# Optimization experiments

Measured on AMD Instinct MI355X. Metric: run time of the kernel, lower is better.

Reference implementation:

```python
import jax, jax.numpy as jnp
import numpy as np

N_NODES = 1500
E = 48000
IN = 128
OUT = 32
HEADS = 4
EDIM = 16


def setup_inputs() -> dict:
    key = jax.random.key(0)
    ks = jax.random.split(key, 16)
    rn = lambda k, shape, s=0.1: jax.random.normal(k, shape, dtype=jnp.float32) * s
    return {
        "x": jax.random.normal(ks[0], (N_NODES, IN), dtype=jnp.float32),
        "edges": jax.random.randint(ks[1], (2, E), 0, N_NODES),
        "edge_feature": jax.random.normal(ks[2], (E, EDIM), dtype=jnp.float32),
        "W1": rn(ks[3], (IN, HEADS * OUT)),
        "att_src1": rn(ks[4], (HEADS, OUT)),
        "att_dst1": rn(ks[5], (HEADS, OUT)),
        "We": rn(ks[6], (EDIM, HEADS * OUT)),
        "att_e": rn(ks[7], (HEADS, OUT)),
        "b1": jnp.zeros((OUT,), jnp.float32),
        "W2": rn(ks[8], (OUT, HEADS * OUT)),
        "att_src2": rn(ks[9], (HEADS, OUT)),
        "att_dst2": rn(ks[10], (HEADS, OUT)),
        "b2": jnp.zeros((OUT,), jnp.float32),
        "fc1_w": rn(ks[11], (2 * OUT, 32)),
        "fc1_b": jnp.zeros((32,), jnp.float32),
        "fc2_w": rn(ks[12], (32, 2)),
        "fc2_b": jnp.zeros((2,), jnp.float32),
    }


def _gat(h, src, dst, n, a_src, a_dst, bias, extra_alpha=None):
    # h: [n, H, C] projected node features; edges j=src -> i=dst (PyG GATConv)
    alpha = (h * a_src).sum(-1)[src] + (h * a_dst).sum(-1)[dst]  # [Etot, H]
    if extra_alpha is not None:
        alpha = alpha + extra_alpha
    alpha = jax.nn.leaky_relu(alpha, negative_slope=0.2)
    m = jax.ops.segment_max(alpha, dst, num_segments=n)  # per-dst softmax (stable)
    e = jnp.exp(alpha - m[dst])
    s = jax.ops.segment_sum(e, dst, num_segments=n)
    w = e / s[dst]  # every node has a self loop -> denom > 0
    out = jax.ops.segment_sum(w[:, :, None] * h[src], dst, num_segments=n)  # [n, H, C]
    return out.mean(axis=1) + bias  # concat=False -> mean over heads


def reference(x, edges, edge_feature, W1, att_src1, att_dst1, We, att_e, b1,
              W2, att_src2, att_dst2, b2, fc1_w, fc1_b, fc2_w, fc2_b):
    n = x.shape[0]
    src0, dst0 = edges[0], edges[1]
    loop = jnp.arange(n, dtype=src0.dtype)
    src = jnp.concatenate([src0, loop])
    dst = jnp.concatenate([dst0, loop])
    # add_self_loops fill_value='mean': self-loop attr = mean of incoming edge attrs
    cnt = jax.ops.segment_sum(jnp.ones_like(dst0, dtype=jnp.float32), dst0, num_segments=n)
    loop_attr = jax.ops.segment_sum(edge_feature, dst0, num_segments=n) / jnp.maximum(cnt, 1.0)[:, None]
    ea = jnp.concatenate([edge_feature, loop_attr], axis=0)  # [E+n, EDIM]

    H, C = att_src1.shape
    # layer 1: GATConv with edge features
    h1 = (x @ W1).reshape(n, H, C)
    extra = ((ea @ We).reshape(-1, H, C) * att_e).sum(-1)  # [E+n, H]
    x1 = _gat(h1, src, dst, n, att_src1, att_dst1, b1, extra)  # [n, OUT]
    # layer 2: GATConv without edge features
    h2 = (x1 @ W2).reshape(n, H, C)
    x2 = _gat(h2, src, dst, n, att_src2, att_dst2, b2)  # [n, OUT]

    # per-edge gather-concat into a (n^2, 2*OUT) buffer; rows >= E stay zero,
    # exactly as the original Python loop leaves them
    pair = jnp.concatenate([x2[src0], x2[dst0]], axis=1)  # [E, 2*OUT]
    x_edges = jnp.zeros((n * n, 2 * C), dtype=x2.dtype).at[jnp.arange(src0.shape[0])].set(pair)
    hcls = jax.nn.relu(x_edges @ fc1_w + fc1_b)
    return jax.nn.softmax(hcls @ fc2_w + fc2_b, axis=1)
```

## Files before the change

kernel.cpp:

```cpp
#include <hip/hip_runtime.h>
#include <cmath>

#define N_NODES 1500
#define NE 48000
#define IN_DIM 128
#define OUT_DIM 32
#define HEADS 4
#define HC 128
#define EDIM 16
#define NBLK 512
#define NTHR 256
#define GSZ (NBLK * NTHR)
#define SLOTS 96
#define NFL4 (((N_NODES * N_NODES - NE) * 2) / 4)
#define F1CNT 300000
#define F2CNT 400500

__device__ __forceinline__ void wt_f(float* p, float v) {
    __hip_atomic_store(p, v, __ATOMIC_RELAXED, __HIP_MEMORY_SCOPE_AGENT);
}
__device__ __forceinline__ void wt_i(int* p, int v) {
    __hip_atomic_store(p, v, __ATOMIC_RELAXED, __HIP_MEMORY_SCOPE_AGENT);
}
__device__ __forceinline__ void wt_f2(float* p, float2 v) {
    unsigned long long u;
    __builtin_memcpy(&u, &v, 8);
    __hip_atomic_store((unsigned long long*)p, u, __ATOMIC_RELAXED, __HIP_MEMORY_SCOPE_AGENT);
}

__device__ __forceinline__ void gsync(int* stripes, int* flag, int epoch) {
    __syncthreads();
    int t = threadIdx.x;
    if (blockIdx.x == 0) {
        if (t < 64) {
            if (t == 0) {
                asm volatile("s_waitcnt vmcnt(0)" ::: "memory");
                __hip_atomic_fetch_add(&stripes[0], 1, __ATOMIC_RELAXED, __HIP_MEMORY_SCOPE_AGENT);
            }
            const int target = NBLK * epoch;
            for (;;) {
                int v = __hip_atomic_load(&stripes[t * 16], __ATOMIC_RELAXED, __HIP_MEMORY_SCOPE_AGENT);
                #pragma unroll
                for (int o = 32; o >= 1; o >>= 1) v += __shfl_down(v, o, 64);
                v = __shfl(v, 0, 64);
                if (v >= target) break;
                __builtin_amdgcn_s_sleep(1);
            }
            if (t == 0)
                __hip_atomic_store(flag, epoch, __ATOMIC_RELAXED, __HIP_MEMORY_SCOPE_AGENT);
        }
    } else {
        if (t == 0) {
            asm volatile("s_waitcnt vmcnt(0)" ::: "memory");
            __hip_atomic_fetch_add(&stripes[(blockIdx.x & 63) * 16], 1,
                                   __ATOMIC_RELAXED, __HIP_MEMORY_SCOPE_AGENT);
            while (__hip_atomic_load(flag, __ATOMIC_RELAXED, __HIP_MEMORY_SCOPE_AGENT) < epoch)
                __builtin_amdgcn_s_sleep(8);
        }
    }
    asm volatile("" ::: "memory");
    __syncthreads();
}

__device__ __forceinline__ float comp4(float4 v, int h) {
    float a = (h & 1) ? v.y : v.x;
    float b = (h & 1) ? v.w : v.z;
    return (h & 2) ? b : a;
}
__device__ __forceinline__ float lk(float a) { return a > 0.f ? a : 0.2f * a; }

template <int MODE>
__device__ __forceinline__ void gat_wave(
        int i, const float* __restrict__ h, const float* __restrict__ asrc,
        const float* __restrict__ adst, const float* __restrict__ ext,
        const int* __restrict__ csr_src, const int* __restrict__ deg,
        const float* __restrict__ bias,
        const float* __restrict__ Wn, const float* __restrict__ a_s2,
        const float* __restrict__ a_d2, float* h2o, float* asrc2,
        float* adst2, float* uvo, int* sns_w, float* swt_w)
{
    const int lane = threadIdx.x & 63;
    const int head = lane >> 4;
    const int p = lane & 15;
    int dg = deg[i]; if (dg > SLOTS) dg = SLOTS;
    const int base = i * SLOTS;
    const float4 ad4 = *(const float4*)&adst[i * 4];
    const float* hb = h + 2 * lane;

    float4 m = make_float4(-INFINITY, -INFINITY, -INFINITY, -INFINITY);
    float4 s = make_float4(0.f, 0.f, 0.f, 0.f);
    float4 sx = make_float4(0.f, 0.f, 0.f, 0.f);
    float2 acc = make_float2(0.f, 0.f);

    for (int pos = 0; pos < dg; pos += 64) {
        int cnt = dg - pos; if (cnt > 64) cnt = 64;
        bool act = lane < cnt;
        int sn = 0;
        float4 al = make_float4(-INFINITY, -INFINITY, -INFINITY, -INFINITY);
        if (act) {
            sn = csr_src[base + pos + lane];
            float4 a4 = *(const float4*)&asrc[sn * 4];
            al = make_float4(a4.x + ad4.x, a4.y + ad4.y, a4.z + ad4.z, a4.w + ad4.w);
            if (MODE == 1) {
                float4 e4 = *(const float4*)&ext[(base + pos + lane) * 4];
                al.x += e4.x; al.y += e4.y; al.z += e4.z; al.w += e4.w;
                sx.x += e4.x; sx.y += e4.y; sx.z += e4.z; sx.w += e4.w;
            }
            al.x = lk(al.x); al.y = lk(al.y); al.z = lk(al.z); al.w = lk(al.w);
        }
        float4 cm = al;
        #pragma unroll
        for (int o = 32; o >= 1; o >>= 1) {
            cm.x = fmaxf(cm.x, __shfl_xor(cm.x, o));
            cm.y = fmaxf(cm.y, __shfl_xor(cm.y, o));
            cm.z = fmaxf(cm.z, __shfl_xor(cm.z, o));
            cm.w = fmaxf(cm.w, __shfl_xor(cm.w, o));
        }
        float4 mn = make_float4(fmaxf(m.x, cm.x), fmaxf(m.y, cm.y),
                                fmaxf(m.z, cm.z), fmaxf(m.w, cm.w));
        float4 r = make_float4(__expf(m.x - mn.x), __expf(m.y - mn.y),
                               __expf(m.z - mn.z), __expf(m.w - mn.w));
        float4 wv4 = make_float4(0.f, 0.f, 0.f, 0.f);
        if (act) {
            wv4.x = __expf(al.x - mn.x); wv4.y = __expf(al.y - mn.y);
            wv4.z = __expf(al.z - mn.z); wv4.w = __expf(al.w - mn.w);
        }
        float4 cs = wv4;
        #pragma unroll
        for (int o = 32; o >= 1; o >>= 1) {
            cs.x += __shfl_xor(cs.x, o); cs.y += __shfl_xor(cs.y, o);
            cs.z += __shfl_xor(cs.z, o); cs.w += __shfl_xor(cs.w, o);
        }
        s = make_float4(s.x * r.x + cs.x, s.y * r.y + cs.y,
                        s.z * r.z + cs.z, s.w * r.w + cs.w);
        float rh = comp4(r, head);
        acc.x *= rh; acc.y *= rh;
        m = mn;
        if (act) {
            sns_w[lane] = sn;
            *(float4*)&swt_w[lane * 4] = wv4;
        }
        int jj = 0;
        for (; jj + 8 <= cnt; jj += 8) {
            int s0 = sns_w[jj], s1 = sns_w[jj+1], s2 = sns_w[jj+2], s3 = sns_w[jj+3];
            int s4 = sns_w[jj+4], s5 = sns_w[jj+5], s6 = sns_w[jj+6], s7 = sns_w[jj+7];
            float w0 = swt_w[(jj)*4+head],   w1 = swt_w[(jj+1)*4+head];
            float w2 = swt_w[(jj+2)*4+head], w3 = swt_w[(jj+3)*4+head];
            float w4 = swt_w[(jj+4)*4+head], w5 = swt_w[(jj+5)*4+head];
            float w6 = swt_w[(jj+6)*4+head], w7 = swt_w[(jj+7)*4+head];
            float2 h0 = *(const float2*)&hb[s0 * HC], h1 = *(const float2*)&hb[s1 * HC];
            float2 h2 = *(const float2*)&hb[s2 * HC], h3 = *(const float2*)&hb[s3 * HC];
            float2 h4 = *(const float2*)&hb[s4 * HC], h5 = *(const float2*)&hb[s5 * HC];
            float2 h6 = *(const float2*)&hb[s6 * HC], h7 = *(const float2*)&hb[s7 * HC];
            acc.x = fmaf(w0, h0.x, acc.x); acc.y = fmaf(w0, h0.y, acc.y);
            acc.x = fmaf(w1, h1.x, acc.x); acc.y = fmaf(w1, h1.y, acc.y);
            acc.x = fmaf(w2, h2.x, acc.x); acc.y = fmaf(w2, h2.y, acc.y);
            acc.x = fmaf(w3, h3.x, acc.x); acc.y = fmaf(w3, h3.y, acc.y);
            acc.x = fmaf(w4, h4.x, acc.x); acc.y = fmaf(w4, h4.y, acc.y);
            acc.x = fmaf(w5, h5.x, acc.x); acc.y = fmaf(w5, h5.y, acc.y);
            acc.x = fmaf(w6, h6.x, acc.x); acc.y = fmaf(w6, h6.y, acc.y);
            acc.x = fmaf(w7, h7.x, acc.x); acc.y = fmaf(w7, h7.y, acc.y);
        }
        for (; jj < cnt; ++jj) {
            int sj = sns_w[jj];
            float wj = swt_w[jj * 4 + head];
            float2 hv = *(const float2*)&hb[sj * HC];
            acc.x = fmaf(wj, hv.x, acc.x);
            acc.y = fmaf(wj, hv.y, acc.y);
        }
    }
    {
        float4 a4 = *(const float4*)&asrc[i * 4];
        float4 al = make_float4(a4.x + ad4.x, a4.y + ad4.y, a4.z + ad4.z, a4.w + ad4.w);
        if (MODE == 1) {
            #pragma unroll
            for (int o = 32; o >= 1; o >>= 1) {
                sx.x += __shfl_xor(sx.x, o); sx.y += __shfl_xor(sx.y, o);
                sx.z += __shfl_xor(sx.z, o); sx.w += __shfl_xor(sx.w, o);
            }
            float invc = 1.f / (float)(dg > 1 ? dg : 1);
            al.x = fmaf(sx.x, invc, al.x); al.y = fmaf(sx.y, invc, al.y);
            al.z = fmaf(sx.z, invc, al.z); al.w = fmaf(sx.w, invc, al.w);
        }
        al.x = lk(al.x); al.y = lk(al.y); al.z = lk(al.z); al.w = lk(al.w);
        float4 mn = make_float4(fmaxf(m.x, al.x), fmaxf(m.y, al.y),
                                fmaxf(m.z, al.z), fmaxf(m.w, al.w));
        float4 r = make_float4(__expf(m.x - mn.x), __expf(m.y - mn.y),
                               __expf(m.z - mn.z), __expf(m.w - mn.w));
        float4 wv4 = make_float4(__expf(al.x - mn.x), __expf(al.y - mn.y),
                                 __expf(al.z - mn.z), __expf(al.w - mn.w));
        s = make_float4(s.x * r.x + wv4.x, s.y * r.y + wv4.y,
                        s.z * r.z + wv4.z, s.w * r.w + wv4.w);
        float rh = comp4(r, head), wh = comp4(wv4, head);
        float2 hv = *(const float2*)&hb[i * HC];
        acc.x = acc.x * rh + wh * hv.x;
        acc.y = acc.y * rh + wh * hv.y;
    }
    float sh = comp4(s, head);
    float2 v = make_float2(acc.x / sh, acc.y / sh);
    v.x += __shfl_xor(v.x, 16); v.y += __shfl_xor(v.y, 16);
    v.x += __shfl_xor(v.x, 32); v.y += __shfl_xor(v.y, 32);
    float2 bp = *(const float2*)&bias[2 * p];
    float2 xr = make_float2(0.25f * v.x + bp.x, 0.25f * v.y + bp.y);

    if (MODE == 1) {
        float2 a2 = make_float2(0.f, 0.f);
        #pragma unroll
        for (int k = 0; k < OUT_DIM; ++k) {
            float xk = __shfl((k & 1) ? xr.y : xr.x, k >> 1);
            float2 wr = *(const float2*)&Wn[k * HC + 2 * lane];
            a2.x = fmaf(xk, wr.x, a2.x);
            a2.y = fmaf(xk, wr.y, a2.y);
        }
        wt_f2(&h2o[i * HC + 2 * lane], a2);
        float2 s2 = *(const float2*)&a_s2[2 * lane];
        float2 d2 = *(const float2*)&a_d2[2 * lane];
        float lps = a2.x * s2.x + a2.y * s2.y;
        float lpd = a2.x * d2.x + a2.y * d2.y;
        #pragma unroll
        for (int o = 8; o >= 1; o >>= 1) {
            lps += __shfl_xor(lps, o);
            lpd += __shfl_xor(lpd, o);
        }
        if (p == 0) {
            wt_f(&asrc2[i * 4 + head], lps);
            wt_f(&adst2[i * 4 + head], lpd);
        }
    } else {
        if (lane < 32) {
            bool isv = lane >= 16;
            int j0 = isv ? (2 * lane - 32) : (2 * lane);
            float2 a2 = make_float2(0.f, 0.f);
            #pragma unroll
            for (int k = 0; k < OUT_DIM; ++k) {
                float xk = __shfl((k & 1) ? xr.y : xr.x, k >> 1);
                int row = isv ? (OUT_DIM + k) : k;
                float2 wr = *(const float2*)&Wn[row * 32 + j0];
                a2.x = fmaf(xk, wr.x, a2.x);
                a2.y = fmaf(xk, wr.y, a2.y);
            }
            wt_f2(&uvo[i * 64 + 2 * lane], a2);
        }
    }
}

__device__ __forceinline__ float4 fill_const(
        const float* fc1b, const float* fc2w, const float* fc2b) {
    float l0 = fc2b[0], l1 = fc2b[1];
    #pragma unroll
    for (int j = 0; j < 32; ++j) {
        float a = fmaxf(fc1b[j], 0.f);
        l0 = fmaf(a, fc2w[2 * j], l0);
        l1 = fmaf(a, fc2w[2 * j + 1], l1);
    }
    float mx = fmaxf(l0, l1);
    float e0 = __expf(l0 - mx), e1 = __expf(l1 - mx);
    float inv = 1.f / (e0 + e1);
    return make_float4(e0 * inv, e1 * inv, e0 * inv, e1 * inv);
}

__global__ __launch_bounds__(NTHR, 2) void k_mega(
    const float* __restrict__ x, const int* __restrict__ edges,
    const float* __restrict__ ef,
    const float* __restrict__ W1, const float* __restrict__ as1, const float* __restrict__ ad1,
    const float* __restrict__ We, const float* __restrict__ ate,
    const float* __restrict__ b1,
    const float* __restrict__ W2, const float* __restrict__ as2, const float* __restrict__ ad2,
    const float* __restrict__ b2,
    const float* __restrict__ fc1w, const float* __restrict__ fc1b,
    const float* __restrict__ fc2w, const float* __restrict__ fc2b,
    float* __restrict__ out,
    float* h1, float* asrc1, float* adst1,
    int* csr_src, float* csr_ext, int* deg,
    float* h2, float* asrc2, float* adst2, float* uv,
    int* stripes, int* flag)
{
    const int t = threadIdx.x;
    const int b = blockIdx.x;
    const int wid = t >> 6;
    const int* src = edges;
    const int* dst = edges + NE;

    __shared__ float P[EDIM * HEADS];
    __shared__ float xs[6 * IN_DIM];
    __shared__ int   sns[4][SLOTS];
    __shared__ float swt[4][SLOTS * 4];

    if (t < EDIM * HEADS) {
        int k = t >> 2, hh = t & 3;
        float a = 0.f;
        #pragma unroll
        for (int c = 0; c < OUT_DIM; ++c)
            a = fmaf(We[k * HC + hh * OUT_DIM + c], ate[hh * OUT_DIM + c], a);
        P[t] = a;
    }
    __syncthreads();

    if (b < 188) {
        int e = b * NTHR + t;
        if (e < NE) {
            int d = dst[e];
            int r = atomicAdd(&deg[d], 1);
            const float4* efp = (const float4*)&ef[e * EDIM];
            float er[16];
            float4 f;
            f = efp[0]; er[0]=f.x; er[1]=f.y; er[2]=f.z; er[3]=f.w;
            f = efp[1]; er[4]=f.x; er[5]=f.y; er[6]=f.z; er[7]=f.w;
            f = efp[2]; er[8]=f.x; er[9]=f.y; er[10]=f.z; er[11]=f.w;
            f = efp[3]; er[12]=f.x; er[13]=f.y; er[14]=f.z; er[15]=f.w;
            float a0=0.f, a1=0.f, a2=0.f, a3=0.f;
            #pragma unroll
            for (int k = 0; k < EDIM; ++k) {
                a0 = fmaf(er[k], P[k*4+0], a0);
                a1 = fmaf(er[k], P[k*4+1], a1);
                a2 = fmaf(er[k], P[k*4+2], a2);
                a3 = fmaf(er[k], P[k*4+3], a3);
            }
            if (r < SLOTS) {
                int slot = d * SLOTS + r;
                wt_i(&csr_src[slot], src[e]);
                wt_f2(&csr_ext[slot * 4],     make_float2(a0, a1));
                wt_f2(&csr_ext[slot * 4 + 2], make_float2(a2, a3));
            }
        }
    } else if (b < 438) {
        int i0 = 6 * (b - 188);
        for (int idx = t; idx < 6 * IN_DIM; idx += NTHR) xs[idx] = x[i0 * IN_DIM + idx];
        __syncthreads();
        int col = t & 127, g = t >> 7;
        float a0 = 0.f, a1 = 0.f, a2 = 0.f;
        for (int k = 0; k < IN_DIM; ++k) {
            float w = W1[k * HC + col];
            a0 = fmaf(xs[(g * 3 + 0) * IN_DIM + k], w, a0);
            a1 = fmaf(xs[(g * 3 + 1) * IN_DIM + k], w, a1);
            a2 = fmaf(xs[(g * 3 + 2) * IN_DIM + k], w, a2);
        }
        float as = as1[col], ad = ad1[col];
        int hh = col >> 5, c = col & 31;
        float av[3] = {a0, a1, a2};
        #pragma unroll
        for (int r = 0; r < 3; ++r) {
            int node = i0 + g * 3 + r;
            wt_f(&h1[node * HC + col], av[r]);
            float ps = av[r] * as, pd = av[r] * ad;
            #pragma unroll
            for (int o = 16; o >= 1; o >>= 1) { ps += __shfl_down(ps, o, 32); pd += __shfl_down(pd, o, 32); }
            if (c == 0) { wt_f(&asrc1[node * 4 + hh], ps); wt_f(&adst1[node * 4 + hh], pd); }
        }
    } else {
        float4 q = fill_const(fc1b, fc2w, fc2b);
        float4* o4 = (float4*)(out + NE * 2);
        for (int idx = (b - 438) * NTHR + t; idx < F1CNT; idx += 74 * NTHR) o4[idx] = q;
    }
    gsync(stripes, flag, 1);

    for (int i = b * 4 + wid; i < N_NODES; i += NBLK * 4)
        gat_wave<1>(i, h1, asrc1, adst1, csr_ext, csr_src, deg, b1,
                    W2, as2, ad2, h2, asrc2, adst2, nullptr,
                    sns[wid], swt[wid]);
    {
        float4 q = fill_const(fc1b, fc2w, fc2b);
        float4* o4 = (float4*)(out + NE * 2);
        for (int idx = F1CNT + b * NTHR + t; idx < F1CNT + F2CNT; idx += GSZ) o4[idx] = q;
    }
    gsync(stripes, flag, 2);

    for (int i = b * 4 + wid; i < N_NODES; i += NBLK * 4)
        gat_wave<2>(i, h2, asrc2, adst2, nullptr, csr_src, deg, b2,
                    fc1w, nullptr, nullptr, nullptr, nullptr, nullptr, uv,
                    sns[wid], swt[wid]);
    {
        float4 q = fill_const(fc1b, fc2w, fc2b);
        float4* o4 = (float4*)(out + NE * 2);
        for (int idx = F1CNT + F2CNT + b * NTHR + t; idx < NFL4; idx += GSZ) o4[idx] = q;
    }
    gsync(stripes, flag, 3);

    {
        int e = b * NTHR + t;
        if (e < NE) {
            int si = src[e], di = dst[e];
            const float4* up = (const float4*)&uv[si * 64];
            const float4* vp = (const float4*)&uv[di * 64 + 32];
            float l0 = fc2b[0], l1 = fc2b[1];
            #pragma unroll
            for (int q = 0; q < 8; ++q) {
                float4 u4 = up[q], v4 = vp[q];
                float a;
                a = fmaxf(u4.x + v4.x + fc1b[4*q+0], 0.f); l0 = fmaf(a, fc2w[8*q+0], l0); l1 = fmaf(a, fc2w[8*q+1], l1);
                a = fmaxf(u4.y + v4.y + fc1b[4*q+1], 0.f); l0 = fmaf(a, fc2w[8*q+2], l0); l1 = fmaf(a, fc2w[8*q+3], l1);
                a = fmaxf(u4.z + v4.z + fc1b[4*q+2], 0.f); l0 = fmaf(a, fc2w[8*q+4], l0); l1 = fmaf(a, fc2w[8*q+5], l1);
                a = fmaxf(u4.w + v4.w + fc1b[4*q+3], 0.f); l0 = fmaf(a, fc2w[8*q+6], l0); l1 = fmaf(a, fc2w[8*q+7], l1);
            }
            float mx = fmaxf(l0, l1);
            float e0 = __expf(l0 - mx), e1 = __expf(l1 - mx);
            float inv = 1.f / (e0 + e1);
            *(float2*)&out[2 * e] = make_float2(e0 * inv, e1 * inv);
        }
    }
}

extern "C" void kernel_launch(void* const* d_in, const int* in_sizes, int n_in,
                              void* d_out, int out_size, void* d_ws, size_t ws_size,
                              hipStream_t stream) {
    (void)in_sizes; (void)n_in; (void)out_size; (void)ws_size;
    const float* x    = (const float*)d_in[0];
    const int*  edges = (const int*)d_in[1];
    const float* ef   = (const float*)d_in[2];
    const float* W1   = (const float*)d_in[3];
    const float* as1  = (const float*)d_in[4];
    const float* ad1  = (const float*)d_in[5];
    const float* We   = (const float*)d_in[6];
    const float* ate  = (const float*)d_in[7];
    const float* b1   = (const float*)d_in[8];
    const float* W2   = (const float*)d_in[9];
    const float* as2  = (const float*)d_in[10];
    const float* ad2  = (const float*)d_in[11];
    const float* b2   = (const float*)d_in[12];
    const float* fc1w = (const float*)d_in[13];
    const float* fc1b = (const float*)d_in[14];
    const float* fc2w = (const float*)d_in[15];
    const float* fc2b = (const float*)d_in[16];
    float* out = (float*)d_out;

    char* w = (char*)d_ws;
    auto alloc = [&](size_t bytes) -> char* {
        char* p = w;
        w += (bytes + 255) & ~(size_t)255;
        return p;
    };
    float* h1      = (float*)alloc((size_t)N_NODES * HC * 4);
    float* asrc1   = (float*)alloc((size_t)N_NODES * HEADS * 4);
    float* adst1   = (float*)alloc((size_t)N_NODES * HEADS * 4);
    int*   csr_src = (int*)  alloc((size_t)N_NODES * SLOTS * 4);
    float* csr_ext = (float*)alloc((size_t)N_NODES * SLOTS * 16);
    float* h2      = (float*)alloc((size_t)N_NODES * HC * 4);
    float* asrc2   = (float*)alloc((size_t)N_NODES * HEADS * 4);
    float* adst2   = (float*)alloc((size_t)N_NODES * HEADS * 4);
    float* uv      = (float*)alloc((size_t)N_NODES * 64 * 4);
    int*   zreg    = (int*)  alloc((size_t)(1536 + 64 * 16 + 16) * 4);
    int*   deg     = zreg;
    int*   stripes = zreg + 1536;
    int*   flag    = zreg + 1536 + 64 * 16;

    hipMemsetAsync(zreg, 0, (size_t)(1536 + 64 * 16 + 16) * 4, stream);
    k_mega<<<NBLK, NTHR, 0, stream>>>(
        x, edges, ef, W1, as1, ad1, We, ate, b1, W2, as2, ad2, b2,
        fc1w, fc1b, fc2w, fc2b, out,
        h1, asrc1, adst1, csr_src, csr_ext, deg,
        h2, asrc2, adst2, uv, stripes, flag);
}
```

Baseline: 142.0 us.

## Split persistent megakernel into four kernels replacing software grid barriers

Replaces the single persistent kernel with custom atomic grid barriers by four ordinary launches: prep, two GAT layers and an edge MLP. Stream ordering now provides the dependencies, so the agent-scope atomic stores and the spin barriers go away and plain or vectorised stores are used instead. The constant-fill of the large output tail is rebalanced across the first three kernels using idle blocks. The cost is extra launch overhead and kernel-boundary drains in place of in-kernel barriers.

Result: faster. 130.5 us (-8.1%).

```diff
diff --git a/kernel.cpp b/kernel.cpp
--- a/kernel.cpp
+++ b/kernel.cpp
@@ -8,59 +8,9 @@
 #define HEADS 4
 #define HC 128
 #define EDIM 16
-#define NBLK 512
-#define NTHR 256
-#define GSZ (NBLK * NTHR)
 #define SLOTS 96
 #define NFL4 (((N_NODES * N_NODES - NE) * 2) / 4)
-#define F1CNT 300000
-#define F2CNT 400500
-
-__device__ __forceinline__ void wt_f(float* p, float v) {
-    __hip_atomic_store(p, v, __ATOMIC_RELAXED, __HIP_MEMORY_SCOPE_AGENT);
-}
-__device__ __forceinline__ void wt_i(int* p, int v) {
-    __hip_atomic_store(p, v, __ATOMIC_RELAXED, __HIP_MEMORY_SCOPE_AGENT);
-}
-__device__ __forceinline__ void wt_f2(float* p, float2 v) {
-    unsigned long long u;
-    __builtin_memcpy(&u, &v, 8);
-    __hip_atomic_store((unsigned long long*)p, u, __ATOMIC_RELAXED, __HIP_MEMORY_SCOPE_AGENT);
-}
-
-__device__ __forceinline__ void gsync(int* stripes, int* flag, int epoch) {
-    __syncthreads();
-    int t = threadIdx.x;
-    if (blockIdx.x == 0) {
-        if (t < 64) {
-            if (t == 0) {
-                asm volatile("s_waitcnt vmcnt(0)" ::: "memory");
-                __hip_atomic_fetch_add(&stripes[0], 1, __ATOMIC_RELAXED, __HIP_MEMORY_SCOPE_AGENT);
-            }
-            const int target = NBLK * epoch;
-            for (;;) {
-                int v = __hip_atomic_load(&stripes[t * 16], __ATOMIC_RELAXED, __HIP_MEMORY_SCOPE_AGENT);
-                #pragma unroll
-                for (int o = 32; o >= 1; o >>= 1) v += __shfl_down(v, o, 64);
-                v = __shfl(v, 0, 64);
-                if (v >= target) break;
-                __builtin_amdgcn_s_sleep(1);
-            }
-            if (t == 0)
-                __hip_atomic_store(flag, epoch, __ATOMIC_RELAXED, __HIP_MEMORY_SCOPE_AGENT);
-        }
-    } else {
-        if (t == 0) {
-            asm volatile("s_waitcnt vmcnt(0)" ::: "memory");
-            __hip_atomic_fetch_add(&stripes[(blockIdx.x & 63) * 16], 1,
-                                   __ATOMIC_RELAXED, __HIP_MEMORY_SCOPE_AGENT);
-            while (__hip_atomic_load(flag, __ATOMIC_RELAXED, __HIP_MEMORY_SCOPE_AGENT) < epoch)
-                __builtin_amdgcn_s_sleep(8);
-        }
-    }
-    asm volatile("" ::: "memory");
-    __syncthreads();
-}
+#define FCH 367000
 
 __device__ __forceinline__ float comp4(float4 v, int h) {
     float a = (h & 1) ? v.y : v.x;
@@ -68,6 +18,21 @@
     return (h & 2) ? b : a;
 }
 __device__ __forceinline__ float lk(float a) { return a > 0.f ? a : 0.2f * a; }
+
+__device__ __forceinline__ float4 fill_const(
+        const float* fc1b, const float* fc2w, const float* fc2b) {
+    float l0 = fc2b[0], l1 = fc2b[1];
+    #pragma unroll
+    for (int j = 0; j < 32; ++j) {
+        float a = fmaxf(fc1b[j], 0.f);
+        l0 = fmaf(a, fc2w[2 * j], l0);
+        l1 = fmaf(a, fc2w[2 * j + 1], l1);
+    }
+    float mx = fmaxf(l0, l1);
+    float e0 = __expf(l0 - mx), e1 = __expf(l1 - mx);
+    float inv = 1.f / (e0 + e1);
+    return make_float4(e0 * inv, e1 * inv, e0 * inv, e1 * inv);
+}
 
 template <int MODE>
 __device__ __forceinline__ void gat_wave(
@@ -212,7 +177,7 @@
             a2.x = fmaf(xk, wr.x, a2.x);
             a2.y = fmaf(xk, wr.y, a2.y);
         }
-        wt_f2(&h2o[i * HC + 2 * lane], a2);
+        *(float2*)&h2o[i * HC + 2 * lane] = a2;
         float2 s2 = *(const float2*)&a_s2[2 * lane];
         float2 d2 = *(const float2*)&a_d2[2 * lane];
         float lps = a2.x * s2.x + a2.y * s2.y;
@@ -223,8 +188,8 @@
             lpd += __shfl_xor(lpd, o);
         }
         if (p == 0) {
-            wt_f(&asrc2[i * 4 + head], lps);
-            wt_f(&adst2[i * 4 + head], lpd);
+            asrc2[i * 4 + head] = lps;
+            adst2[i * 4 + head] = lpd;
         }
     } else {
         if (lane < 32) {
@@ -239,65 +204,41 @@
                 a2.x = fmaf(xk, wr.x, a2.x);
                 a2.y = fmaf(xk, wr.y, a2.y);
             }
-            wt_f2(&uvo[i * 64 + 2 * lane], a2);
-        }
-    }
-}
-
-__device__ __forceinline__ float4 fill_const(
-        const float* fc1b, const float* fc2w, const float* fc2b) {
-    float l0 = fc2b[0], l1 = fc2b[1];
-    #pragma unroll
-    for (int j = 0; j < 32; ++j) {
-        float a = fmaxf(fc1b[j], 0.f);
-        l0 = fmaf(a, fc2w[2 * j], l0);
-        l1 = fmaf(a, fc2w[2 * j + 1], l1);
-    }
-    float mx = fmaxf(l0, l1);
-    float e0 = __expf(l0 - mx), e1 = __expf(l1 - mx);
-    float inv = 1.f / (e0 + e1);
-    return make_float4(e0 * inv, e1 * inv, e0 * inv, e1 * inv);
-}
-
-__global__ __launch_bounds__(NTHR, 2) void k_mega(
+            *(float2*)&uvo[i * 64 + 2 * lane] = a2;
+        }
+    }
+}
+
+__global__ __launch_bounds__(256) void k_prep(
     const float* __restrict__ x, const int* __restrict__ edges,
     const float* __restrict__ ef,
-    const float* __restrict__ W1, const float* __restrict__ as1, const float* __restrict__ ad1,
-    const float* __restrict__ We, const float* __restrict__ ate,
-    const float* __restrict__ b1,
-    const float* __restrict__ W2, const float* __restrict__ as2, const float* __restrict__ ad2,
-    const float* __restrict__ b2,
-    const float* __restrict__ fc1w, const float* __restrict__ fc1b,
-    const float* __restrict__ fc2w, const float* __restrict__ fc2b,
+    const float* __restrict__ W1, const float* __restrict__ as1,
+    const float* __restrict__ ad1, const float* __restrict__ We,
+    const float* __restrict__ ate,
+    const float* __restrict__ fc1b, const float* __restrict__ fc2w,
+    const float* __restrict__ fc2b,
     float* __restrict__ out,
-    float* h1, float* asrc1, float* adst1,
-    int* csr_src, float* csr_ext, int* deg,
-    float* h2, float* asrc2, float* adst2, float* uv,
-    int* stripes, int* flag)
+    float* __restrict__ h1, float* __restrict__ asrc1, float* __restrict__ adst1,
+    int* __restrict__ csr_src, float* __restrict__ csr_ext, int* __restrict__ deg)
 {
     const int t = threadIdx.x;
     const int b = blockIdx.x;
-    const int wid = t >> 6;
     const int* src = edges;
     const int* dst = edges + NE;
-
     __shared__ float P[EDIM * HEADS];
     __shared__ float xs[6 * IN_DIM];
-    __shared__ int   sns[4][SLOTS];
-    __shared__ float swt[4][SLOTS * 4];
-
-    if (t < EDIM * HEADS) {
-        int k = t >> 2, hh = t & 3;
-        float a = 0.f;
-        #pragma unroll
-        for (int c = 0; c < OUT_DIM; ++c)
-            a = fmaf(We[k * HC + hh * OUT_DIM + c], ate[hh * OUT_DIM + c], a);
-        P[t] = a;
-    }
-    __syncthreads();
 
     if (b < 188) {
-        int e = b * NTHR + t;
+        if (t < EDIM * HEADS) {
+            int k = t >> 2, hh = t & 3;
+            float a = 0.f;
+            #pragma unroll
+            for (int c = 0; c < OUT_DIM; ++c)
+                a = fmaf(We[k * HC + hh * OUT_DIM + c], ate[hh * OUT_DIM + c], a);
+            P[t] = a;
+        }
+        __syncthreads();
+        int e = b * 256 + t;
         if (e < NE) {
             int d = dst[e];
             int r = atomicAdd(&deg[d], 1);
@@ -318,14 +259,13 @@
             }
             if (r < SLOTS) {
                 int slot = d * SLOTS + r;
-                wt_i(&csr_src[slot], src[e]);
-                wt_f2(&csr_ext[slot * 4],     make_float2(a0, a1));
-                wt_f2(&csr_ext[slot * 4 + 2], make_float2(a2, a3));
+                csr_src[slot] = src[e];
+                *(float4*)&csr_ext[slot * 4] = make_float4(a0, a1, a2, a3);
             }
         }
     } else if (b < 438) {
         int i0 = 6 * (b - 188);
-        for (int idx = t; idx < 6 * IN_DIM; idx += NTHR) xs[idx] = x[i0 * IN_DIM + idx];
+        for (int idx = t; idx < 6 * IN_DIM; idx += 256) xs[idx] = x[i0 * IN_DIM + idx];
         __syncthreads();
         int col = t & 127, g = t >> 7;
         float a0 = 0.f, a1 = 0.f, a2 = 0.f;
@@ -341,63 +281,78 @@
         #pragma unroll
         for (int r = 0; r < 3; ++r) {
             int node = i0 + g * 3 + r;
-            wt_f(&h1[node * HC + col], av[r]);
+            h1[node * HC + col] = av[r];
             float ps = av[r] * as, pd = av[r] * ad;
             #pragma unroll
             for (int o = 16; o >= 1; o >>= 1) { ps += __shfl_down(ps, o, 32); pd += __shfl_down(pd, o, 32); }
-            if (c == 0) { wt_f(&asrc1[node * 4 + hh], ps); wt_f(&adst1[node * 4 + hh], pd); }
+            if (c == 0) { asrc1[node * 4 + hh] = ps; adst1[node * 4 + hh] = pd; }
         }
     } else {
         float4 q = fill_const(fc1b, fc2w, fc2b);
         float4* o4 = (float4*)(out + NE * 2);
-        for (int idx = (b - 438) * NTHR + t; idx < F1CNT; idx += 74 * NTHR) o4[idx] = q;
-    }
-    gsync(stripes, flag, 1);
-
-    for (int i = b * 4 + wid; i < N_NODES; i += NBLK * 4)
-        gat_wave<1>(i, h1, asrc1, adst1, csr_ext, csr_src, deg, b1,
-                    W2, as2, ad2, h2, asrc2, adst2, nullptr,
-                    sns[wid], swt[wid]);
-    {
+        for (int idx = (b - 438) * 256 + t; idx < FCH; idx += 74 * 256) o4[idx] = q;
+    }
+}
+
+template <int MODE>
+__global__ __launch_bounds__(256) void k_gat(
+    const float* __restrict__ h, const float* __restrict__ asrc,
+    const float* __restrict__ adst, const float* __restrict__ ext,
+    const int* __restrict__ csr_src, const int* __restrict__ deg,
+    const float* __restrict__ bias, const float* __restrict__ Wn,
+    const float* __restrict__ a_s2, const float* __restrict__ a_d2,
+    const float* __restrict__ fc1b, const float* __restrict__ fc2w,
+    const float* __restrict__ fc2b, float* __restrict__ out,
+    float* __restrict__ h2o, float* __restrict__ asrc2,
+    float* __restrict__ adst2, float* __restrict__ uvo)
+{
+    const int t = threadIdx.x;
+    const int b = blockIdx.x;
+    const int wid = t >> 6;
+    __shared__ int   sns[4][SLOTS];
+    __shared__ float swt[4][SLOTS * 4];
+
+    if (b < 375) {
+        int i = b * 4 + wid;
+        gat_wave<MODE>(i, h, asrc, adst, ext, csr_src, deg, bias,
+                       Wn, a_s2, a_d2, h2o, asrc2, adst2, uvo,
+                       sns[wid], swt[wid]);
+    } else {
         float4 q = fill_const(fc1b, fc2w, fc2b);
         float4* o4 = (float4*)(out + NE * 2);
-        for (int idx = F1CNT + b * NTHR + t; idx < F1CNT + F2CNT; idx += GSZ) o4[idx] = q;
-    }
-    gsync(stripes, flag, 2);
-
-    for (int i = b * 4 + wid; i < N_NODES; i += NBLK * 4)
-        gat_wave<2>(i, h2, asrc2, adst2, nullptr, csr_src, deg, b2,
-                    fc1w, nullptr, nullptr, nullptr, nullptr, nullptr, uv,
-                    sns[wid], swt[wid]);
-    {
-        float4 q = fill_const(fc1b, fc2w, fc2b);
-        float4* o4 = (float4*)(out + NE * 2);
-        for (int idx = F1CNT + F2CNT + b * NTHR + t; idx < NFL4; idx += GSZ) o4[idx] = q;
-    }
-    gsync(stripes, flag, 3);
-
-    {
-        int e = b * NTHR + t;
-        if (e < NE) {
-            int si = src[e], di = dst[e];
-            const float4* up = (const float4*)&uv[si * 64];
-            const float4* vp = (const float4*)&uv[di * 64 + 32];
-            float l0 = fc2b[0], l1 = fc2b[1];
-            #pragma unroll
-            for (int q = 0; q < 8; ++q) {
-                float4 u4 = up[q], v4 = vp[q];
-                float a;
-                a = fmaxf(u4.x + v4.x + fc1b[4*q+0], 0.f); l0 = fmaf(a, fc2w[8*q+0], l0); l1 = fmaf(a, fc2w[8*q+1], l1);
-                a = fmaxf(u4.y + v4.y + fc1b[4*q+1], 0.f); l0 = fmaf(a, fc2w[8*q+2], l0); l1 = fmaf(a, fc2w[8*q+3], l1);
-                a = fmaxf(u4.z + v4.z + fc1b[4*q+2], 0.f); l0 = fmaf(a, fc2w[8*q+4], l0); l1 = fmaf(a, fc2w[8*q+5], l1);
-                a = fmaxf(u4.w + v4.w + fc1b[4*q+3], 0.f); l0 = fmaf(a, fc2w[8*q+6], l0); l1 = fmaf(a, fc2w[8*q+7], l1);
-            }
-            float mx = fmaxf(l0, l1);
-            float e0 = __expf(l0 - mx), e1 = __expf(l1 - mx);
-            float inv = 1.f / (e0 + e1);
-            *(float2*)&out[2 * e] = make_float2(e0 * inv, e1 * inv);
-        }
-    }
+        int start = (MODE == 1) ? FCH : 2 * FCH;
+        int end   = (MODE == 1) ? 2 * FCH : NFL4;
+        for (int idx = start + (b - 375) * 256 + t; idx < end; idx += 137 * 256)
+            o4[idx] = q;
+    }
+}
+
+__global__ __launch_bounds__(256) void k_mlp(
+    const int* __restrict__ edges, const float* __restrict__ uv,
+    const float* __restrict__ fc1b, const float* __restrict__ fc2w,
+    const float* __restrict__ fc2b, float* __restrict__ out)
+{
+    const int* src = edges;
+    const int* dst = edges + NE;
+    int e = blockIdx.x * 256 + threadIdx.x;
+    if (e >= NE) return;
+    int si = src[e], di = dst[e];
+    const float4* up = (const float4*)&uv[si * 64];
+    const float4* vp = (const float4*)&uv[di * 64 + 32];
+    float l0 = fc2b[0], l1 = fc2b[1];
+    #pragma unroll
+    for (int q = 0; q < 8; ++q) {
+        float4 u4 = up[q], v4 = vp[q];
+        float a;
+        a = fmaxf(u4.x + v4.x + fc1b[4*q+0], 0.f); l0 = fmaf(a, fc2w[8*q+0], l0); l1 = fmaf(a, fc2w[8*q+1], l1);
+        a = fmaxf(u4.y + v4.y + fc1b[4*q+1], 0.f); l0 = fmaf(a, fc2w[8*q+2], l0); l1 = fmaf(a, fc2w[8*q+3], l1);
+        a = fmaxf(u4.z + v4.z + fc1b[4*q+2], 0.f); l0 = fmaf(a, fc2w[8*q+4], l0); l1 = fmaf(a, fc2w[8*q+5], l1);
+        a = fmaxf(u4.w + v4.w + fc1b[4*q+3], 0.f); l0 = fmaf(a, fc2w[8*q+6], l0); l1 = fmaf(a, fc2w[8*q+7], l1);
+    }
+    float mx = fmaxf(l0, l1);
+    float e0 = __expf(l0 - mx), e1 = __expf(l1 - mx);
+    float inv = 1.f / (e0 + e1);
+    *(float2*)&out[2 * e] = make_float2(e0 * inv, e1 * inv);
 }
 
 extern "C" void kernel_launch(void* const* d_in, const int* in_sizes, int n_in,
@@ -438,15 +393,17 @@
     float* asrc2   = (float*)alloc((size_t)N_NODES * HEADS * 4);
     float* adst2   = (float*)alloc((size_t)N_NODES * HEADS * 4);
     float* uv      = (float*)alloc((size_t)N_NODES * 64 * 4);
-    int*   zreg    = (int*)  alloc((size_t)(1536 + 64 * 16 + 16) * 4);
-    int*   deg     = zreg;
-    int*   stripes = zreg + 1536;
-    int*   flag    = zreg + 1536 + 64 * 16;
-
-    hipMemsetAsync(zreg, 0, (size_t)(1536 + 64 * 16 + 16) * 4, stream);
-    k_mega<<<NBLK, NTHR, 0, stream>>>(
-        x, edges, ef, W1, as1, ad1, We, ate, b1, W2, as2, ad2, b2,
-        fc1w, fc1b, fc2w, fc2b, out,
-        h1, asrc1, adst1, csr_src, csr_ext, deg,
-        h2, asrc2, adst2, uv, stripes, flag);
-}
+    int*   deg     = (int*)  alloc((size_t)N_NODES * 4);
+
+    hipMemsetAsync(deg, 0, (size_t)N_NODES * 4, stream);
+    k_prep<<<512, 256, 0, stream>>>(x, edges, ef, W1, as1, ad1, We, ate,
+                                    fc1b, fc2w, fc2b, out,
+                                    h1, asrc1, adst1, csr_src, csr_ext, deg);
+    k_gat<1><<<512, 256, 0, stream>>>(h1, asrc1, adst1, csr_ext, csr_src, deg,
+                                      b1, W2, as2, ad2, fc1b, fc2w, fc2b, out,
+                                      h2, asrc2, adst2, nullptr);
+    k_gat<2><<<512, 256, 0, stream>>>(h2, asrc2, adst2, nullptr, csr_src, deg,
+                                      b2, fc1w, nullptr, nullptr, fc1b, fc2w, fc2b, out,
+                                      nullptr, nullptr, nullptr, uv);
+    k_mlp<<<188, 256, 0, stream>>>(edges, uv, fc1b, fc2w, fc2b, out);
+}
```
